# Performance work log

Measured on AMD Instinct MI355X. Metric: run time of the kernel, lower is better.

Reference implementation:

```python
import jax, jax.numpy as jnp
import numpy as np

B, V_IN, V_OUT, F_IN, F_OUT, N_CP = 100000, 128, 128, 512, 512, 16
DIM_H = max(V_IN, V_OUT)  # hidden_vectors=None -> max(dim_vectors_in, dim_vectors_out)
EPS = 1e-8


def setup_inputs() -> dict:
    key = jax.random.key(0)
    ks = jax.random.split(key, 9)
    u = lambda k, shape, scale: jax.random.uniform(k, shape, jnp.float32, -scale, scale)
    wh_k = 1.0 / np.sqrt(V_IN).astype(np.float32)
    wu_k = 1.0 / np.sqrt(DIM_H + N_CP).astype(np.float32)
    f_in = DIM_H + N_CP + F_IN  # 656
    kf = 1.0 / np.sqrt(f_in).astype(np.float32)
    kg = 1.0 / np.sqrt(F_OUT).astype(np.float32)
    return {
        "feats": jax.random.normal(ks[0], (B, F_IN), jnp.float32),
        "vectors": jax.random.normal(ks[1], (B, V_IN, 3), jnp.float32),
        "Wh": u(ks[2], (V_IN, DIM_H), wh_k),
        "Wcp": u(ks[3], (V_IN, 2 * N_CP), wh_k),
        "Wu": u(ks[4], (DIM_H + N_CP, V_OUT), wu_k),
        "Wf": u(ks[5], (f_in, F_OUT), kf),      # torch Linear weight, stored (in,out)
        "bf": u(ks[6], (F_OUT,), kf),
        "Wg": u(ks[7], (F_OUT, V_OUT), kg),
        "bg": u(ks[8], (V_OUT,), kg),
    }


def reference(feats, vectors, Wh, Wcp, Wu, Wf, bf, Wg, bg):
    # vectors: [b, v_in, 3]; mix vector channels (matmul acts per xyz component c)
    Vh = jnp.einsum('bvc,vh->bhc', vectors, Wh)            # [b, dim_h, 3]
    # cross-product features
    Vcp = jnp.einsum('bvc,vp->bpc', vectors, Wcp)          # [b, 2*n_cp, 3]
    cp = jnp.cross(Vcp[:, :N_CP], Vcp[:, N_CP:])           # [b, n_cp, 3]
    Vh = jnp.concatenate([Vh, cp], axis=1)                 # [b, dim_h+n_cp, 3]
    Vu = jnp.einsum('bkc,ko->boc', Vh, Wu)                 # [b, v_out, 3]
    # clamped L2 norm over xyz
    sh = jnp.sqrt(jnp.maximum(jnp.sum(Vh * Vh, axis=-1), EPS))  # [b, dim_h+n_cp]
    s = jnp.concatenate([feats, sh], axis=1)               # [b, dim_h+n_cp+f_in]
    feats_out = jax.nn.silu(s @ Wf + bf)                   # [b, f_out]
    gating = feats_out @ Wg + bg                           # [b, v_out]
    vectors_out = jax.nn.sigmoid(gating)[..., None] * Vu   # [b, v_out, 3]
    return feats_out, vectors_out
```

## Files before the change

kernel.cpp:

```cpp
#include <hip/hip_runtime.h>

#define BATCH 100000
#define M3 300000
#define VECBASE 51200000
#define KP 704

typedef float fl4  __attribute__((ext_vector_type(4)));
typedef float f32x4 __attribute__((ext_vector_type(4)));
typedef short s16x4 __attribute__((ext_vector_type(4)));
typedef short s16x8 __attribute__((ext_vector_type(8)));

__device__ __forceinline__ short f2bf(float f) {
  unsigned int u = __float_as_uint(f);
  u += 0x7fffu + ((u >> 16) & 1u);
  return (short)(u >> 16);
}
__device__ __forceinline__ float bf2f(short s) {
  return __uint_as_float(((unsigned int)(unsigned short)s) << 16);
}
__device__ __forceinline__ s16x8 pack8(fl4 a, fl4 b) {
  s16x8 o;
  o[0] = f2bf(a[0]); o[1] = f2bf(a[1]); o[2] = f2bf(a[2]); o[3] = f2bf(a[3]);
  o[4] = f2bf(b[0]); o[5] = f2bf(b[1]); o[6] = f2bf(b[2]); o[7] = f2bf(b[3]);
  return o;
}
__device__ __forceinline__ void glds16(const void* g, void* l) {
  __builtin_amdgcn_global_load_lds((const __attribute__((address_space(1))) void*)g,
                                   (__attribute__((address_space(3))) void*)l, 16, 0, 0);
}

__global__ __launch_bounds__(256) void prep_w(
    const float* __restrict__ feats, const float* __restrict__ Wh,
    const float* __restrict__ Wcp, const float* __restrict__ Wu,
    const float* __restrict__ Wf, const float* __restrict__ Wg,
    short* __restrict__ Ab, short* __restrict__ WB1, short* __restrict__ WuTp,
    short* __restrict__ WfT, short* __restrict__ WgT) {
  const int tid = blockIdx.x * 256 + threadIdx.x;
  const int stride = gridDim.x * 256;
  for (int i = tid; i < 6400000; i += stride) {
    int b = i >> 6, kk = (i & 63) * 8;
    fl4 v0 = *reinterpret_cast<const fl4*>(&feats[(size_t)b * 512 + kk]);
    fl4 v1 = *reinterpret_cast<const fl4*>(&feats[(size_t)b * 512 + kk + 4]);
    *(s16x8*)&Ab[(size_t)b * KP + kk] = pack8(v0, v1);
  }
  for (int gid = tid; gid < 466944; gid += stride) {
    if (gid < 20480) {
      int n = gid >> 7, k = gid & 127;
      WB1[gid] = f2bf(n < 128 ? Wh[k * 128 + n] : Wcp[k * 32 + (n - 128)]);
    } else if (gid < 40960) {
      int i = gid - 20480;
      int o = i / 160, k = i - o * 160;
      WuTp[i] = k < 144 ? f2bf(Wu[k * 128 + o]) : (short)0;
    } else if (gid < 401408) {
      int i = gid - 40960;
      int n = i / KP, k = i - n * KP;
      WfT[i] = k < 656 ? f2bf(Wf[k * 512 + n]) : (short)0;
    } else {
      int i = gid - 401408;
      int n = i >> 9, k = i & 511;
      WgT[i] = f2bf(Wg[k * 128 + n]);
    }
  }
}

__global__ __launch_bounds__(256) void geo_fused(
    const float* __restrict__ vecs, const short* __restrict__ WB1,
    const short* __restrict__ WuTp, short* __restrict__ Ab,
    short* __restrict__ Vub) {
  __shared__ __align__(16) short U[192 * 168];
  const int t = threadIdx.x;
  const int b0 = blockIdx.x * 64;
  const int row0 = blockIdx.x * 192;

#pragma unroll
  for (int it = 0; it < 8; ++it) {
    int fi = (it * 256 + t) * 12;
    int bl = fi / 384;
    int rem = fi - bl * 384;
    int v0 = rem / 3;
    int b = b0 + bl;
    fl4 x = (fl4){0.f, 0.f, 0.f, 0.f}, y = x, z = x;
    if (b < BATCH) {
      const float* p = &vecs[(size_t)b * 384 + rem];
      x = *(const fl4*)p; y = *(const fl4*)(p + 4); z = *(const fl4*)(p + 8);
    }
    float vc[3][4] = {{x[0], x[3], y[2], z[1]},
                      {x[1], y[0], y[3], z[2]},
                      {x[2], y[1], z[0], z[3]}};
#pragma unroll
    for (int c = 0; c < 3; ++c) {
      int row = bl * 3 + c;
      s16x4 q;
#pragma unroll
      for (int e = 0; e < 4; ++e) q[e] = f2bf(vc[c][e]);
      int off = (row << 8) + (v0 << 1);
      *(s16x4*)((char*)U + (off ^ ((row & 7) << 4))) = q;
    }
  }
  __syncthreads();

  const int lane = t & 63, wv = t >> 6;
  const int wr = wv >> 1, wc = wv & 1;
  const int lr = lane & 15, lk = lane >> 4;

  {
    f32x4 acc[6][5];
#pragma unroll
    for (int i = 0; i < 6; ++i)
#pragma unroll
      for (int j = 0; j < 5; ++j) acc[i][j] = (f32x4){0.f, 0.f, 0.f, 0.f};
#pragma unroll
    for (int kk = 0; kk < 4; ++kk) {
      s16x8 af[6], bq[5];
#pragma unroll
      for (int mi = 0; mi < 6; ++mi) {
        int row = wr * 96 + mi * 16 + lr;
        int off = (row << 8) + (kk << 6) + (lk << 4);
        af[mi] = *(const s16x8*)((const char*)U + (off ^ ((row & 7) << 4)));
      }
#pragma unroll
      for (int ni = 0; ni < 5; ++ni)
        bq[ni] = *reinterpret_cast<const s16x8*>(
            &WB1[(wc * 80 + ni * 16 + lr) * 128 + (kk << 5) + (lk << 3)]);
      __builtin_amdgcn_s_setprio(1);
#pragma unroll
      for (int mi = 0; mi < 6; ++mi)
#pragma unroll
        for (int ni = 0; ni < 5; ++ni)
          acc[mi][ni] = __builtin_amdgcn_mfma_f32_16x16x32_bf16(af[mi], bq[ni], acc[mi][ni], 0, 0, 0);
      __builtin_amdgcn_s_setprio(0);
    }
    __syncthreads();
#pragma unroll
    for (int mi = 0; mi < 6; ++mi)
#pragma unroll
      for (int ni = 0; ni < 5; ++ni) {
        int col = wc * 80 + ni * 16 + lr;
#pragma unroll
        for (int r = 0; r < 4; ++r) {
          int row = wr * 96 + mi * 16 + lk * 4 + r;
          U[row * 168 + col] = f2bf(acc[mi][ni][r]);
        }
      }
  }
  __syncthreads();

  {
    int bl = t >> 2, pj = t & 3;
    int gb = b0 + bl;
    float shcp[4];
#pragma unroll
    for (int q = 0; q < 4; ++q) {
      int p = pj * 4 + q;
      float ax = bf2f(U[(bl * 3 + 0) * 168 + 128 + p]);
      float ay = bf2f(U[(bl * 3 + 1) * 168 + 128 + p]);
      float az = bf2f(U[(bl * 3 + 2) * 168 + 128 + p]);
      float bx = bf2f(U[(bl * 3 + 0) * 168 + 144 + p]);
      float by = bf2f(U[(bl * 3 + 1) * 168 + 144 + p]);
      float bz = bf2f(U[(bl * 3 + 2) * 168 + 144 + p]);
      float cx = ay * bz - az * by;
      float cy = az * bx - ax * bz;
      float cz = ax * by - ay * bx;
      U[(bl * 3 + 0) * 168 + 128 + p] = f2bf(cx);
      U[(bl * 3 + 1) * 168 + 128 + p] = f2bf(cy);
      U[(bl * 3 + 2) * 168 + 128 + p] = f2bf(cz);
      U[(bl * 3 + 0) * 168 + 144 + p] = 0;
      U[(bl * 3 + 1) * 168 + 144 + p] = 0;
      U[(bl * 3 + 2) * 168 + 144 + p] = 0;
      shcp[q] = sqrtf(fmaxf(cx * cx + cy * cy + cz * cz, 1e-8f));
    }
    if (gb < BATCH) {
#pragma unroll
      for (int q = 0; q < 4; ++q)
        Ab[(size_t)gb * KP + 512 + 128 + pj * 4 + q] = f2bf(shcp[q]);
#pragma unroll
      for (int z = 0; z < 12; ++z)
        Ab[(size_t)gb * KP + 512 + 144 + pj * 12 + z] = 0;
    }
  }
  {
    int bl = t >> 2, kq = t & 3;
    int gb = b0 + bl;
    if (gb < BATCH) {
#pragma unroll
      for (int j = 0; j < 4; ++j) {
        int k = kq * 32 + j * 8;
        s16x8 r0 = *(const s16x8*)&U[(bl * 3 + 0) * 168 + k];
        s16x8 r1 = *(const s16x8*)&U[(bl * 3 + 1) * 168 + k];
        s16x8 r2 = *(const s16x8*)&U[(bl * 3 + 2) * 168 + k];
        s16x8 o;
#pragma unroll
        for (int e = 0; e < 8; ++e) {
          float x = bf2f(r0[e]), y = bf2f(r1[e]), z = bf2f(r2[e]);
          o[e] = f2bf(sqrtf(fmaxf(x * x + y * y + z * z, 1e-8f)));
        }
        *(s16x8*)&Ab[(size_t)gb * KP + 512 + k] = o;
      }
    }
  }
  __syncthreads();

  {
    f32x4 acc2[6][4];
#pragma unroll
    for (int i = 0; i < 6; ++i)
#pragma unroll
      for (int j = 0; j < 4; ++j) acc2[i][j] = (f32x4){0.f, 0.f, 0.f, 0.f};
#pragma unroll
    for (int kk = 0; kk < 5; ++kk) {
      s16x8 af[6], bq[4];
#pragma unroll
      for (int mi = 0; mi < 6; ++mi) {
        int row = wr * 96 + mi * 16 + lr;
        af[mi] = *(const s16x8*)&U[row * 168 + (kk << 5) + (lk << 3)];
      }
#pragma unroll
      for (int ni = 0; ni < 4; ++ni)
        bq[ni] = *reinterpret_cast<const s16x8*>(
            &WuTp[(wc * 64 + ni * 16 + lr) * 160 + (kk << 5) + (lk << 3)]);
      __builtin_amdgcn_s_setprio(1);
#pragma unroll
      for (int mi = 0; mi < 6; ++mi)
#pragma unroll
        for (int ni = 0; ni < 4; ++ni)
          acc2[mi][ni] = __builtin_amdgcn_mfma_f32_16x16x32_bf16(af[mi], bq[ni], acc2[mi][ni], 0, 0, 0);
      __builtin_amdgcn_s_setprio(0);
    }
#pragma unroll
    for (int mi = 0; mi < 6; ++mi)
#pragma unroll
      for (int ni = 0; ni < 4; ++ni) {
        int col = wc * 64 + ni * 16 + lr;
#pragma unroll
        for (int r = 0; r < 4; ++r) {
          int row = row0 + wr * 96 + mi * 16 + lk * 4 + r;
          if (row < M3) Vub[(size_t)row * 128 + col] = f2bf(acc2[mi][ni][r]);
        }
      }
  }
}

__global__ __launch_bounds__(256) void gemm_feats(
    const short* __restrict__ Ab, const short* __restrict__ WfT,
    const float* __restrict__ bfv, float* __restrict__ out,
    short* __restrict__ fob) {
  const int bid = blockIdx.x;
  const int swz = (bid & 7) * 391 + (bid >> 3);
  const int mt = swz >> 2, nt = swz & 3;
  const int row0 = mt << 7, n0 = nt << 7;
  const int t = threadIdx.x;
  const int lane = t & 63, wv = t >> 6;
  const int wr = wv >> 1, wc = wv & 1;
  const int lr = lane & 15, lk = lane >> 4;

  __shared__ __align__(16) short As[2][128 * 64];
  __shared__ __align__(16) short Bs[2][128 * 64];

  const short* srcA[4];
  const short* srcB[4];
  int dofs[4];
#pragma unroll
  for (int j = 0; j < 4; ++j) {
    int cid = j * 256 + t;
    int row = cid >> 3, ch = cid & 7;
    int chs = ch ^ (row & 7);
    srcA[j] = &Ab[(size_t)min(row0 + row, BATCH - 1) * KP + chs * 8];
    srcB[j] = &WfT[(size_t)(n0 + row) * KP + chs * 8];
    dofs[j] = cid * 8;
  }

  f32x4 acc[4][4];
#pragma unroll
  for (int i = 0; i < 4; ++i)
#pragma unroll
    for (int j = 0; j < 4; ++j) acc[i][j] = (f32x4){0.f, 0.f, 0.f, 0.f};

  auto STAGE = [&](int buf, int ks) {
    const int k0 = ks << 6;
#pragma unroll
    for (int j = 0; j < 4; ++j) glds16(srcA[j] + k0, &As[buf][dofs[j]]);
#pragma unroll
    for (int j = 0; j < 4; ++j) glds16(srcB[j] + k0, &Bs[buf][dofs[j]]);
  };
  auto COMPUTE = [&](int buf) {
#pragma unroll
    for (int kk = 0; kk < 2; ++kk) {
      s16x8 af[4], bq[4];
#pragma unroll
      for (int mi = 0; mi < 4; ++mi) {
        int rw = wr * 64 + mi * 16 + lr;
        af[mi] = *(const s16x8*)&As[buf][rw * 64 + (((kk << 2) + lk) ^ (rw & 7)) * 8];
      }
#pragma unroll
      for (int ni = 0; ni < 4; ++ni) {
        int rw = wc * 64 + ni * 16 + lr;
        bq[ni] = *(const s16x8*)&Bs[buf][rw * 64 + (((kk << 2) + lk) ^ (rw & 7)) * 8];
      }
      __builtin_amdgcn_s_setprio(1);
#pragma unroll
      for (int mi = 0; mi < 4; ++mi)
#pragma unroll
        for (int ni = 0; ni < 4; ++ni)
          acc[mi][ni] = __builtin_amdgcn_mfma_f32_16x16x32_bf16(af[mi], bq[ni], acc[mi][ni], 0, 0, 0);
      __builtin_amdgcn_s_setprio(0);
    }
  };

  STAGE(0, 0);
  __syncthreads();
  for (int ks = 0; ks < 11; ++ks) {
    if (ks + 1 < 11) STAGE((ks + 1) & 1, ks + 1);
    COMPUTE(ks & 1);
    __syncthreads();
  }

#pragma unroll
  for (int ni = 0; ni < 4; ++ni) {
    int col = n0 + wc * 64 + ni * 16 + lr;
    float bb = bfv[col];
#pragma unroll
    for (int mi = 0; mi < 4; ++mi) {
      int rbase = row0 + wr * 64 + mi * 16 + lk * 4;
#pragma unroll
      for (int rr = 0; rr < 4; ++rr) {
        int gr = rbase + rr;
        if (gr < BATCH) {
          float x = acc[mi][ni][rr] + bb;
          float y = x / (1.f + __expf(-x));
          out[(size_t)gr * 512 + col] = y;
          fob[(size_t)gr * 512 + col] = f2bf(y);
        }
      }
    }
  }
}

__global__ __launch_bounds__(256) void gemm_gate(
    const short* __restrict__ fob, const short* __restrict__ WgT,
    const float* __restrict__ bg, const short* __restrict__ Vub,
    float* __restrict__ out) {
  const int bid = blockIdx.x;
  const int xcd = bid & 7, bidx = bid >> 3;
  const int swz = (xcd < 6 ? xcd * 98 : 6 * 98 + (xcd - 6) * 97) + bidx;
  const int row0 = swz << 7;
  const int t = threadIdx.x;
  const int lane = t & 63, wv = t >> 6;
  const int wr = wv >> 1, wc = wv & 1;
  const int lr = lane & 15, lk = lane >> 4;

  __shared__ __align__(16) short As[2][128 * 64];
  __shared__ __align__(16) short Bs[2][128 * 64];

  const short* srcA[4];
  const short* srcB[4];
  int dofs[4];
#pragma unroll
  for (int j = 0; j < 4; ++j) {
    int cid = j * 256 + t;
    int row = cid >> 3, ch = cid & 7;
    int chs = ch ^ (row & 7);
    srcA[j] = &fob[(size_t)min(row0 + row, BATCH - 1) * 512 + chs * 8];
    srcB[j] = &WgT[(size_t)row * 512 + chs * 8];
    dofs[j] = cid * 8;
  }

  f32x4 acc[4][4];
#pragma unroll
  for (int i = 0; i < 4; ++i)
#pragma unroll
    for (int j = 0; j < 4; ++j) acc[i][j] = (f32x4){0.f, 0.f, 0.f, 0.f};

  auto STAGE = [&](int buf, int ks) {
    const int k0 = ks << 6;
#pragma unroll
    for (int j = 0; j < 4; ++j) glds16(srcA[j] + k0, &As[buf][dofs[j]]);
#pragma unroll
    for (int j = 0; j < 4; ++j) glds16(srcB[j] + k0, &Bs[buf][dofs[j]]);
  };
  auto COMPUTE = [&](int buf) {
#pragma unroll
    for (int kk = 0; kk < 2; ++kk) {
      s16x8 af[4], bq[4];
#pragma unroll
      for (int mi = 0; mi < 4; ++mi) {
        int rw = wr * 64 + mi * 16 + lr;
        af[mi] = *(const s16x8*)&As[buf][rw * 64 + (((kk << 2) + lk) ^ (rw & 7)) * 8];
      }
#pragma unroll
      for (int ni = 0; ni < 4; ++ni) {
        int rw = wc * 64 + ni * 16 + lr;
        bq[ni] = *(const s16x8*)&Bs[buf][rw * 64 + (((kk << 2) + lk) ^ (rw & 7)) * 8];
      }
      __builtin_amdgcn_s_setprio(1);
#pragma unroll
      for (int mi = 0; mi < 4; ++mi)
#pragma unroll
        for (int ni = 0; ni < 4; ++ni)
          acc[mi][ni] = __builtin_amdgcn_mfma_f32_16x16x32_bf16(af[mi], bq[ni], acc[mi][ni], 0, 0, 0);
      __builtin_amdgcn_s_setprio(0);
    }
  };

  STAGE(0, 0);
  __syncthreads();
  for (int ks = 0; ks < 8; ++ks) {
    if (ks + 1 < 8) STAGE((ks + 1) & 1, ks + 1);
    COMPUTE(ks & 1);
    __syncthreads();
  }

#pragma unroll
  for (int ni = 0; ni < 4; ++ni) {
    int col = wc * 64 + ni * 16 + lr;
    float bb = bg[col];
#pragma unroll
    for (int mi = 0; mi < 4; ++mi) {
      int rbase = row0 + wr * 64 + mi * 16 + lk * 4;
#pragma unroll
      for (int rr = 0; rr < 4; ++rr) {
        int gr = rbase + rr;
        if (gr < BATCH) {
          float x = acc[mi][ni][rr] + bb;
          float gate = 1.f / (1.f + __expf(-x));
          size_t vb = (size_t)(3 * gr) * 128 + col;
          float* po = &out[VECBASE + ((size_t)gr * 128 + col) * 3];
          po[0] = gate * bf2f(Vub[vb]);
          po[1] = gate * bf2f(Vub[vb + 128]);
          po[2] = gate * bf2f(Vub[vb + 256]);
        }
      }
    }
  }
}

extern "C" void kernel_launch(void* const* d_in, const int* in_sizes, int n_in,
                              void* d_out, int out_size, void* d_ws, size_t ws_size,
                              hipStream_t stream) {
  const float* feats = (const float*)d_in[0];
  const float* vecs  = (const float*)d_in[1];
  const float* Wh    = (const float*)d_in[2];
  const float* Wcp   = (const float*)d_in[3];
  const float* Wu    = (const float*)d_in[4];
  const float* Wf    = (const float*)d_in[5];
  const float* bfv   = (const float*)d_in[6];
  const float* Wg    = (const float*)d_in[7];
  const float* bg    = (const float*)d_in[8];
  float* out = (float*)d_out;

  char* ws = (char*)d_ws;
  short* Ab   = (short*)ws;
  short* Vub  = (short*)(ws + 140800000);
  short* fob  = (short*)(ws + 217600000);
  short* WfT  = (short*)(ws + 320000000);
  short* WgT  = (short*)(ws + 320720896);
  short* WB1  = (short*)(ws + 320851968);
  short* WuTp = (short*)(ws + 320892928);

  hipLaunchKernelGGL(prep_w,     dim3(2048), dim3(256), 0, stream,
                     feats, Wh, Wcp, Wu, Wf, Wg, Ab, WB1, WuTp, WfT, WgT);
  hipLaunchKernelGGL(geo_fused,  dim3(1563), dim3(256), 0, stream,
                     vecs, WB1, WuTp, Ab, Vub);
  hipLaunchKernelGGL(gemm_feats, dim3(3128), dim3(256), 0, stream,
                     Ab, WfT, bfv, out, fob);
  hipLaunchKernelGGL(gemm_gate,  dim3(782),  dim3(256), 0, stream,
                     fob, WgT, bg, Vub, out);
}
```

Baseline: 529.5 us.

## Triple-buffer GEMM K-loop with vmcnt-gated barriers and LDS-staged coalesced epilogue

Both GEMM kernels move from double-buffered BK=64 tiles to triple-buffered BK=32 tiles, two stages ahead. Hand-written s_waitcnt vmcnt/s_barrier asm replaces __syncthreads, so each barrier waits only for the oldest stage's loads and global-to-LDS traffic overlaps more with MFMA work. The feats GEMM epilogue also stages SiLU outputs through LDS in 32-row chunks, giving vectorised row-contiguous float and bf16 stores instead of scattered scalar ones. Risks are more barriers per K step, a fragile vmcnt count tied to the number of loads issued per stage, and extra syncs in the epilogue.

```diff
diff --git a/kernel.cpp b/kernel.cpp
--- a/kernel.cpp
+++ b/kernel.cpp
@@ -28,6 +28,8 @@
   __builtin_amdgcn_global_load_lds((const __attribute__((address_space(1))) void*)g,
                                    (__attribute__((address_space(3))) void*)l, 16, 0, 0);
 }
+#define WAITBAR(N) asm volatile("s_waitcnt vmcnt(" #N ")\ns_barrier" ::: "memory")
+#define RAWBAR()   asm volatile("s_barrier" ::: "memory")
 
 __global__ __launch_bounds__(256) void prep_w(
     const float* __restrict__ feats, const float* __restrict__ Wh,
@@ -253,17 +255,17 @@
   const int wr = wv >> 1, wc = wv & 1;
   const int lr = lane & 15, lk = lane >> 4;
 
-  __shared__ __align__(16) short As[2][128 * 64];
-  __shared__ __align__(16) short Bs[2][128 * 64];
-
-  const short* srcA[4];
-  const short* srcB[4];
-  int dofs[4];
-#pragma unroll
-  for (int j = 0; j < 4; ++j) {
+  __shared__ __align__(16) short As[3][128 * 32];
+  __shared__ __align__(16) short Bs[3][128 * 32];
+
+  const short* srcA[2];
+  const short* srcB[2];
+  int dofs[2];
+#pragma unroll
+  for (int j = 0; j < 2; ++j) {
     int cid = j * 256 + t;
-    int row = cid >> 3, ch = cid & 7;
-    int chs = ch ^ (row & 7);
+    int row = cid >> 2, ch = cid & 3;
+    int chs = ch ^ ((row >> 1) & 3);
     srcA[j] = &Ab[(size_t)min(row0 + row, BATCH - 1) * KP + chs * 8];
     srcB[j] = &WfT[(size_t)(n0 + row) * KP + chs * 8];
     dofs[j] = cid * 8;
@@ -276,62 +278,80 @@
     for (int j = 0; j < 4; ++j) acc[i][j] = (f32x4){0.f, 0.f, 0.f, 0.f};
 
   auto STAGE = [&](int buf, int ks) {
-    const int k0 = ks << 6;
-#pragma unroll
-    for (int j = 0; j < 4; ++j) glds16(srcA[j] + k0, &As[buf][dofs[j]]);
-#pragma unroll
-    for (int j = 0; j < 4; ++j) glds16(srcB[j] + k0, &Bs[buf][dofs[j]]);
+    const int k0 = ks << 5;
+#pragma unroll
+    for (int j = 0; j < 2; ++j) glds16(srcA[j] + k0, &As[buf][dofs[j]]);
+#pragma unroll
+    for (int j = 0; j < 2; ++j) glds16(srcB[j] + k0, &Bs[buf][dofs[j]]);
   };
   auto COMPUTE = [&](int buf) {
-#pragma unroll
-    for (int kk = 0; kk < 2; ++kk) {
-      s16x8 af[4], bq[4];
-#pragma unroll
-      for (int mi = 0; mi < 4; ++mi) {
-        int rw = wr * 64 + mi * 16 + lr;
-        af[mi] = *(const s16x8*)&As[buf][rw * 64 + (((kk << 2) + lk) ^ (rw & 7)) * 8];
-      }
-#pragma unroll
-      for (int ni = 0; ni < 4; ++ni) {
-        int rw = wc * 64 + ni * 16 + lr;
-        bq[ni] = *(const s16x8*)&Bs[buf][rw * 64 + (((kk << 2) + lk) ^ (rw & 7)) * 8];
-      }
-      __builtin_amdgcn_s_setprio(1);
-#pragma unroll
-      for (int mi = 0; mi < 4; ++mi)
-#pragma unroll
-        for (int ni = 0; ni < 4; ++ni)
-          acc[mi][ni] = __builtin_amdgcn_mfma_f32_16x16x32_bf16(af[mi], bq[ni], acc[mi][ni], 0, 0, 0);
-      __builtin_amdgcn_s_setprio(0);
-    }
+    s16x8 af[4], bq[4];
+#pragma unroll
+    for (int mi = 0; mi < 4; ++mi) {
+      int rw = wr * 64 + mi * 16 + lr;
+      af[mi] = *(const s16x8*)&As[buf][rw * 32 + (lk ^ ((rw >> 1) & 3)) * 8];
+    }
+#pragma unroll
+    for (int ni = 0; ni < 4; ++ni) {
+      int rw = wc * 64 + ni * 16 + lr;
+      bq[ni] = *(const s16x8*)&Bs[buf][rw * 32 + (lk ^ ((rw >> 1) & 3)) * 8];
+    }
+    __builtin_amdgcn_s_setprio(1);
+#pragma unroll
+    for (int mi = 0; mi < 4; ++mi)
+#pragma unroll
+      for (int ni = 0; ni < 4; ++ni)
+        acc[mi][ni] = __builtin_amdgcn_mfma_f32_16x16x32_bf16(af[mi], bq[ni], acc[mi][ni], 0, 0, 0);
+    __builtin_amdgcn_s_setprio(0);
   };
 
   STAGE(0, 0);
-  __syncthreads();
-  for (int ks = 0; ks < 11; ++ks) {
-    if (ks + 1 < 11) STAGE((ks + 1) & 1, ks + 1);
-    COMPUTE(ks & 1);
+  STAGE(1, 1);
+  for (int ks = 0; ks < 22; ++ks) {
+    if (ks + 2 < 22) STAGE((ks + 2) % 3, ks + 2);
+    if (ks < 20)      WAITBAR(8);
+    else if (ks == 20) WAITBAR(4);
+    else               WAITBAR(0);
+    COMPUTE(ks % 3);
+    RAWBAR();
+  }
+
+  float* Ls = (float*)&As[0][0];
+#pragma unroll
+  for (int g = 0; g < 4; ++g) {
+    if (wr == (g >> 1)) {
+      int miB = (g & 1) * 2;
+#pragma unroll
+      for (int m2 = 0; m2 < 2; ++m2) {
+#pragma unroll
+        for (int ni = 0; ni < 4; ++ni) {
+          int colL = wc * 64 + ni * 16 + lr;
+          float bb = bfv[n0 + colL];
+#pragma unroll
+          for (int rr = 0; rr < 4; ++rr) {
+            int rowL = m2 * 16 + lk * 4 + rr;
+            float x = acc[miB + m2][ni][rr] + bb;
+            Ls[rowL * 128 + colL] = x / (1.f + __expf(-x));
+          }
+        }
+      }
+    }
     __syncthreads();
-  }
-
-#pragma unroll
-  for (int ni = 0; ni < 4; ++ni) {
-    int col = n0 + wc * 64 + ni * 16 + lr;
-    float bb = bfv[col];
-#pragma unroll
-    for (int mi = 0; mi < 4; ++mi) {
-      int rbase = row0 + wr * 64 + mi * 16 + lk * 4;
-#pragma unroll
-      for (int rr = 0; rr < 4; ++rr) {
-        int gr = rbase + rr;
-        if (gr < BATCH) {
-          float x = acc[mi][ni][rr] + bb;
-          float y = x / (1.f + __expf(-x));
-          out[(size_t)gr * 512 + col] = y;
-          fob[(size_t)gr * 512 + col] = f2bf(y);
-        }
-      }
-    }
+    {
+      int rowL = t >> 3, seg = t & 7;
+      int grow = row0 + g * 32 + rowL;
+      if (grow < BATCH) {
+        const float* p = &Ls[rowL * 128 + seg * 16];
+        fl4 a = *(const fl4*)p, b = *(const fl4*)(p + 4);
+        fl4 c = *(const fl4*)(p + 8), d = *(const fl4*)(p + 12);
+        float* po = &out[(size_t)grow * 512 + n0 + seg * 16];
+        *(fl4*)po = a; *(fl4*)(po + 4) = b; *(fl4*)(po + 8) = c; *(fl4*)(po + 12) = d;
+        short* pf = &fob[(size_t)grow * 512 + n0 + seg * 16];
+        *(s16x8*)pf = pack8(a, b);
+        *(s16x8*)(pf + 8) = pack8(c, d);
+      }
+    }
+    __syncthreads();
   }
 }
 
@@ -348,17 +368,17 @@
   const int wr = wv >> 1, wc = wv & 1;
   const int lr = lane & 15, lk = lane >> 4;
 
-  __shared__ __align__(16) short As[2][128 * 64];
-  __shared__ __align__(16) short Bs[2][128 * 64];
-
-  const short* srcA[4];
-  const short* srcB[4];
-  int dofs[4];
-#pragma unroll
-  for (int j = 0; j < 4; ++j) {
+  __shared__ __align__(16) short As[3][128 * 32];
+  __shared__ __align__(16) short Bs[3][128 * 32];
+
+  const short* srcA[2];
+  const short* srcB[2];
+  int dofs[2];
+#pragma unroll
+  for (int j = 0; j < 2; ++j) {
     int cid = j * 256 + t;
-    int row = cid >> 3, ch = cid & 7;
-    int chs = ch ^ (row & 7);
+    int row = cid >> 2, ch = cid & 3;
+    int chs = ch ^ ((row >> 1) & 3);
     srcA[j] = &fob[(size_t)min(row0 + row, BATCH - 1) * 512 + chs * 8];
     srcB[j] = &WgT[(size_t)row * 512 + chs * 8];
     dofs[j] = cid * 8;
@@ -371,42 +391,42 @@
     for (int j = 0; j < 4; ++j) acc[i][j] = (f32x4){0.f, 0.f, 0.f, 0.f};
 
   auto STAGE = [&](int buf, int ks) {
-    const int k0 = ks << 6;
-#pragma unroll
-    for (int j = 0; j < 4; ++j) glds16(srcA[j] + k0, &As[buf][dofs[j]]);
-#pragma unroll
-    for (int j = 0; j < 4; ++j) glds16(srcB[j] + k0, &Bs[buf][dofs[j]]);
+    const int k0 = ks << 5;
+#pragma unroll
+    for (int j = 0; j < 2; ++j) glds16(srcA[j] + k0, &As[buf][dofs[j]]);
+#pragma unroll
+    for (int j = 0; j < 2; ++j) glds16(srcB[j] + k0, &Bs[buf][dofs[j]]);
   };
   auto COMPUTE = [&](int buf) {
-#pragma unroll
-    for (int kk = 0; kk < 2; ++kk) {
-      s16x8 af[4], bq[4];
-#pragma unroll
-      for (int mi = 0; mi < 4; ++mi) {
-        int rw = wr * 64 + mi * 16 + lr;
-        af[mi] = *(const s16x8*)&As[buf][rw * 64 + (((kk << 2) + lk) ^ (rw & 7)) * 8];
-      }
-#pragma unroll
-      for (int ni = 0; ni < 4; ++ni) {
-        int rw = wc * 64 + ni * 16 + lr;
-        bq[ni] = *(const s16x8*)&Bs[buf][rw * 64 + (((kk << 2) + lk) ^ (rw & 7)) * 8];
-      }
-      __builtin_amdgcn_s_setprio(1);
-#pragma unroll
-      for (int mi = 0; mi < 4; ++mi)
-#pragma unroll
-        for (int ni = 0; ni < 4; ++ni)
-          acc[mi][ni] = __builtin_amdgcn_mfma_f32_16x16x32_bf16(af[mi], bq[ni], acc[mi][ni], 0, 0, 0);
-      __builtin_amdgcn_s_setprio(0);
-    }
+    s16x8 af[4], bq[4];
+#pragma unroll
+    for (int mi = 0; mi < 4; ++mi) {
+      int rw = wr * 64 + mi * 16 + lr;
+      af[mi] = *(const s16x8*)&As[buf][rw * 32 + (lk ^ ((rw >> 1) & 3)) * 8];
+    }
+#pragma unroll
+    for (int ni = 0; ni < 4; ++ni) {
+      int rw = wc * 64 + ni * 16 + lr;
+      bq[ni] = *(const s16x8*)&Bs[buf][rw * 32 + (lk ^ ((rw >> 1) & 3)) * 8];
+    }
+    __builtin_amdgcn_s_setprio(1);
+#pragma unroll
+    for (int mi = 0; mi < 4; ++mi)
+#pragma unroll
+      for (int ni = 0; ni < 4; ++ni)
+        acc[mi][ni] = __builtin_amdgcn_mfma_f32_16x16x32_bf16(af[mi], bq[ni], acc[mi][ni], 0, 0, 0);
+    __builtin_amdgcn_s_setprio(0);
   };
 
   STAGE(0, 0);
-  __syncthreads();
-  for (int ks = 0; ks < 8; ++ks) {
-    if (ks + 1 < 8) STAGE((ks + 1) & 1, ks + 1);
-    COMPUTE(ks & 1);
-    __syncthreads();
+  STAGE(1, 1);
+  for (int ks = 0; ks < 16; ++ks) {
+    if (ks + 2 < 16) STAGE((ks + 2) % 3, ks + 2);
+    if (ks < 14)      WAITBAR(8);
+    else if (ks == 14) WAITBAR(4);
+    else               WAITBAR(0);
+    COMPUTE(ks % 3);
+    RAWBAR();
   }
 
 #pragma unroll
```

New measurement: 513.9 us. 1.03x faster.
